# Kernel optimization log

Hardware: AMD Instinct MI355X
Metric: run time of the kernel (lower is better)

## Reference

```python
import jax, jax.numpy as jnp
import numpy as np


def _fft2c(x, axes):
    # fftshift(fft2(ifftshift(x), norm='ortho'))
    return jnp.fft.fftshift(
        jnp.fft.fft2(jnp.fft.ifftshift(x, axes=axes), axes=axes, norm='ortho'),
        axes=axes)


def _warp(img, flow):
    # img: [Nx,Ny] complex, flow: [Nx,Ny,2] (displacements along x,y)
    # Dense equivalent of the sparse bilinear motion matrix apply.
    Nx, Ny = img.shape
    gx = jnp.arange(Nx, dtype=flow.dtype)[:, None]
    gy = jnp.arange(Ny, dtype=flow.dtype)[None, :]
    x = jnp.clip(gx + flow[:, :, 0], 0.0, Nx - 1)
    y = jnp.clip(gy + flow[:, :, 1], 0.0, Ny - 1)
    x0 = jnp.clip(jnp.floor(x), 0, Nx - 2).astype(jnp.int32)
    y0 = jnp.clip(jnp.floor(y), 0, Ny - 2).astype(jnp.int32)
    wx = x - x0
    wy = y - y0
    x1 = x0 + 1
    y1 = y0 + 1
    v00 = img[x0, y0]
    v01 = img[x0, y1]
    v10 = img[x1, y0]
    v11 = img[x1, y1]
    return ((1 - wx) * (1 - wy)) * v00 + ((1 - wx) * wy) * v01 \
         + (wx * (1 - wy)) * v10 + (wx * wy) * v11


def setup_inputs() -> dict:
    key = jax.random.key(0)
    k = jax.random.split(key, 6)
    Nx, Ny, Nc, Nt = 256, 256, 16, 24
    return {
        'image_real': jax.random.normal(k[0], (Nx, Ny), dtype=jnp.float32),
        'image_imag': jax.random.normal(k[1], (Nx, Ny), dtype=jnp.float32),
        'mask': jax.random.uniform(k[2], (Nx, Ny, Nc, Nt), dtype=jnp.float32),
        'smaps_real': jax.random.normal(k[3], (Nx, Ny, Nc), dtype=jnp.float32),
        'smaps_imag': jax.random.normal(k[4], (Nx, Ny, Nc), dtype=jnp.float32),
        'flow': jax.random.normal(k[5], (Nx, Ny, 2, Nt), dtype=jnp.float32) * 2.0,
    }


def reference(image_real, image_imag, mask, smaps_real, smaps_imag, flow):
    img = image_real + 1j * image_imag            # [Nx,Ny]
    smaps = smaps_real + 1j * smaps_imag          # [Nx,Ny,Nc]
    flow_t = jnp.moveaxis(flow, -1, 0)            # [Nt,Nx,Ny,2]
    warped = jax.vmap(_warp, in_axes=(None, 0))(img, flow_t)   # [Nt,Nx,Ny]
    coil = warped[:, :, :, None] * smaps[None]    # [Nt,Nx,Ny,Nc]
    k = _fft2c(coil, axes=(1, 2))                 # [Nt,Nx,Ny,Nc]
    mask_t = jnp.moveaxis(mask, -1, 0)            # [Nt,Nx,Ny,Nc]
    out = jnp.sum(k * mask_t, axis=0)             # [Nx,Ny,Nc] complex
    # stack real/imag for a real-valued output (complex not in dtype enum)
    return jnp.stack([out.real, out.imag], axis=0)  # [2,Nx,Ny,Nc]
```

## Files before the change

### kernel.cpp

```cpp
#include <hip/hip_runtime.h>
#include <math.h>

#define NCD 16
#define NTD 24
#define NPIX 65536

struct c32 { float x, y; };

__device__ __forceinline__ c32 cadd(c32 a, c32 b){ return {a.x+b.x, a.y+b.y}; }
__device__ __forceinline__ c32 csub(c32 a, c32 b){ return {a.x-b.x, a.y-b.y}; }
__device__ __forceinline__ c32 cmul(c32 a, c32 b){ return {a.x*b.x - a.y*b.y, a.x*b.y + a.y*b.x}; }
__device__ __forceinline__ c32 cnegi(c32 a){ return {a.y, -a.x}; }

__device__ __forceinline__ unsigned short f2h(float f) {
  return __builtin_bit_cast(unsigned short, (_Float16)f);
}
__device__ __forceinline__ float h2f(unsigned short s) {
  return (float)__builtin_bit_cast(_Float16, s);
}

__constant__ float W16R_[16] = {
  1.0f, 0.9238795325f, 0.7071067812f, 0.3826834324f,
  0.0f,-0.3826834324f,-0.7071067812f,-0.9238795325f,
 -1.0f,-0.9238795325f,-0.7071067812f,-0.3826834324f,
  0.0f, 0.3826834324f, 0.7071067812f, 0.9238795325f };
__constant__ float W16I_[16] = {
  0.0f,-0.3826834324f,-0.7071067812f,-0.9238795325f,
 -1.0f,-0.9238795325f,-0.7071067812f,-0.3826834324f,
  0.0f, 0.3826834324f, 0.7071067812f, 0.9238795325f,
  1.0f, 0.9238795325f, 0.7071067812f, 0.3826834324f };

__device__ __forceinline__ int revmap(int p) { return ((p & 3) << 2) | (p >> 2); }

__device__ __forceinline__ void dft16(c32 v[16]) {
  c32 y[16];
#pragma unroll
  for (int j = 0; j < 4; ++j) {
    c32 a = v[j], b = v[j+4], c = v[j+8], d = v[j+12];
    c32 t0 = cadd(a,c), t1 = csub(a,c), t2 = cadd(b,d), t3 = cnegi(csub(b,d));
    y[j] = cadd(t0,t2);
    if (j == 0) {
      y[4]  = cadd(t1,t3);
      y[8]  = csub(t0,t2);
      y[12] = csub(t1,t3);
    } else {
      c32 w1 = {W16R_[j],        W16I_[j]};
      c32 w2 = {W16R_[(2*j)&15], W16I_[(2*j)&15]};
      c32 w3 = {W16R_[(3*j)&15], W16I_[(3*j)&15]};
      y[4+j]  = cmul(cadd(t1,t3), w1);
      y[8+j]  = cmul(csub(t0,t2), w2);
      y[12+j] = cmul(csub(t1,t3), w3);
    }
  }
#pragma unroll
  for (int q = 0; q < 4; ++q) {
    c32 a = y[4*q], b = y[4*q+1], c = y[4*q+2], d = y[4*q+3];
    c32 t0 = cadd(a,c), t1 = csub(a,c), t2 = cadd(b,d), t3 = cnegi(csub(b,d));
    v[4*q+0] = cadd(t0,t2);
    v[4*q+1] = cadd(t1,t3);
    v[4*q+2] = csub(t0,t2);
    v[4*q+3] = csub(t1,t3);
  }
}

__device__ __forceinline__ void fft256(c32 v[16], const c32 tw[16], c32* lds,
                                       int g, int lane) {
  dft16(v);
#pragma unroll
  for (int p = 0; p < 16; ++p) v[p] = cmul(v[p], tw[p]);
  __syncthreads();
#pragma unroll
  for (int p = 0; p < 16; ++p) {
    int k1 = revmap(p);
    lds[g*256 + k1*16 + (lane ^ k1)] = v[p];
  }
  __syncthreads();
#pragma unroll
  for (int j = 0; j < 16; ++j)
    v[j] = lds[g*256 + lane*16 + (j ^ lane)];
  dft16(v);
}

__global__ __launch_bounds__(256) void kS(const float* __restrict__ sre,
                                          const float* __restrict__ sim,
                                          c32* __restrict__ smapsT) {
  __shared__ float lre[16*260];
  __shared__ float lim[16*260];
  int nx = blockIdx.x, tid = threadIdx.x;
#pragma unroll
  for (int it = 0; it < 16; ++it) {
    int e = it*256 + tid;
    int ny = e >> 4, c = e & 15;
    lre[c*260 + ny] = sre[(size_t)nx*4096 + e];
    lim[c*260 + ny] = sim[(size_t)nx*4096 + e];
  }
  __syncthreads();
#pragma unroll
  for (int c = 0; c < 16; ++c) {
    c32 v = { lre[c*260 + tid], lim[c*260 + tid] };
    smapsT[(size_t)c*NPIX + nx*256 + tid] = v;
  }
}

__global__ __launch_bounds__(256) void kW(const float* __restrict__ ire,
                                          const float* __restrict__ iim,
                                          const float* __restrict__ flow,
                                          c32* __restrict__ w) {
  __shared__ float fl[256*49];
  int nx = blockIdx.x, tid = threadIdx.x;
  const float* src = flow + (size_t)nx*12288;
#pragma unroll
  for (int it = 0; it < 48; ++it) {
    int e = it*256 + tid;
    fl[(e/48)*49 + (e%48)] = src[e];
  }
  __syncthreads();
  int ny = tid;
  float s = ((nx + ny) & 1) ? -1.0f : 1.0f;
  for (int t = 0; t < NTD; ++t) {
    float fx = fl[ny*49 + t];
    float fy = fl[ny*49 + 24 + t];
    float xf = fminf(fmaxf((float)nx + fx, 0.0f), 255.0f);
    float yf = fminf(fmaxf((float)ny + fy, 0.0f), 255.0f);
    float x0f = fminf(floorf(xf), 254.0f);
    float y0f = fminf(floorf(yf), 254.0f);
    int i00 = (int)x0f * 256 + (int)y0f;
    float wx = xf - x0f, wy = yf - y0f;
    float w00 = (1.f-wx)*(1.f-wy), w01 = (1.f-wx)*wy;
    float w10 = wx*(1.f-wy),       w11 = wx*wy;
    float re = w00*ire[i00] + w01*ire[i00+1] + w10*ire[i00+256] + w11*ire[i00+257];
    float im = w00*iim[i00] + w01*iim[i00+1] + w10*iim[i00+256] + w11*iim[i00+257];
    c32 v = { re*s, im*s };
    w[(size_t)t*NPIX + nx*256 + ny] = v;
  }
}

__global__ __launch_bounds__(256) void kM(const float* __restrict__ mask,
                                          unsigned int* __restrict__ maskTh,
                                          int t0, int chunkT) {
  __shared__ unsigned short lm[256*49];
  int ky = blockIdx.x, c0 = blockIdx.y*2, tid = threadIdx.x;
  int nct = 2*chunkT;
  int total = 256*nct;
  for (int e = tid; e < total; e += 256) {
    int kx = e / nct, ctl = e - kx*nct;
    int hi = (ctl >= chunkT) ? 1 : 0;
    int cc = c0 + hi;
    int tt = t0 + ctl - hi*chunkT;
    lm[kx*49 + ctl] = f2h(mask[(size_t)kx*98304 + ky*384 + cc*24 + tt]);
  }
  __syncthreads();
  int wtotal = nct*128;
  for (int e = tid; e < wtotal; e += 256) {
    int ctl = e >> 7;
    int posh = (e & 127) * 2;
    int hi = (ctl >= chunkT) ? 1 : 0;
    int cc = c0 + hi;
    int ltt = ctl - hi*chunkT;
    int kxa = ((posh & 15) << 4) | (posh >> 4);
    int kxb = (((posh+1) & 15) << 4) | ((posh+1) >> 4);
    unsigned int a = lm[kxa*49 + ctl], b = lm[kxb*49 + ctl];
    size_t base = (((((size_t)ltt*256 + ky)*16 + cc) << 8) + posh) >> 1;
    maskTh[base] = a | (b << 16);
  }
}

__global__ __launch_bounds__(256) void kA(const c32* __restrict__ w,
                                          const c32* __restrict__ smapsT,
                                          unsigned int* __restrict__ Y1h, int t0) {
  __shared__ c32 lds[4096];
  __shared__ unsigned int stage[4096];
  int tid = threadIdx.x, g = tid >> 4, lane = tid & 15;
  int lt = blockIdx.y, t = t0 + lt;
  int nx0 = blockIdx.x*16, nx = nx0 + g;
  int c0 = blockIdx.z*4;

  c32 wr[16];
  const c32* wrow = w + (size_t)t*NPIX + nx*256;
#pragma unroll
  for (int n1 = 0; n1 < 16; ++n1) wr[n1] = wrow[n1*16 + lane];

  c32 tw[16];
#pragma unroll
  for (int p = 0; p < 16; ++p) {
    int k1 = revmap(p);
    float ang = -6.283185307179586f * (float)(lane * k1) * (1.0f/256.0f);
    float sv, cv; __sincosf(ang, &sv, &cv);
    tw[p].x = cv; tw[p].y = sv;
  }

  for (int ci = 0; ci < 4; ++ci) {
    int c = c0 + ci;
    const c32* srow = smapsT + (size_t)c*NPIX + nx*256;
    c32 v[16];
#pragma unroll
    for (int n1 = 0; n1 < 16; ++n1) v[n1] = cmul(wr[n1], srow[n1*16 + lane]);
    fft256(v, tw, lds, g, lane);
#pragma unroll
    for (int p = 0; p < 16; ++p) {
      int ky = lane + 16*revmap(p);
      unsigned int pk = (unsigned int)f2h(v[p].x)
                      | ((unsigned int)f2h(v[p].y) << 16);
      stage[ky*16 + (g ^ lane)] = pk;
    }
    __syncthreads();
    unsigned int* dst = Y1h + (((size_t)lt*16 + c) << 16) + nx0;
#pragma unroll
    for (int it = 0; it < 16; ++it) {
      int e = it*256 + tid;
      int ky = e >> 4, j = e & 15;
      dst[(size_t)ky*256 + j] = stage[ky*16 + (j ^ (ky & 15))];
    }
  }
}

__global__ __launch_bounds__(256) void kB(const unsigned int* __restrict__ Y1h,
                                          const unsigned int* __restrict__ maskTh,
                                          float* __restrict__ out,
                                          int chunkT, int accum) {
  __shared__ c32 lds[4096];
  int tid = threadIdx.x, g = tid >> 4, lane = tid & 15;
  int ci = g & 3, tp = g >> 2;
  int cq = blockIdx.x, ky = blockIdx.y;
  int c = cq*4 + ci;

  c32 tw[16];
#pragma unroll
  for (int p = 0; p < 16; ++p) {
    int k1 = revmap(p);
    float ang = -6.283185307179586f * (float)(lane * k1) * (1.0f/256.0f);
    float sv, cv; __sincosf(ang, &sv, &cv);
    tw[p].x = cv; tw[p].y = sv;
  }

  c32 acc[16];
#pragma unroll
  for (int p = 0; p < 16; ++p) { acc[p].x = 0.f; acc[p].y = 0.f; }
  float wsc = (((lane + ky) & 1) ? -1.0f : 1.0f) * (1.0f/256.0f);

  int iters = (chunkT + 3) >> 2;
  for (int ii = 0; ii < iters; ++ii) {
    int lt = tp + 4*ii;
    bool act = lt < chunkT;
    int lts = act ? lt : 0;
    const unsigned int* row = Y1h + ((size_t)(lts*16 + c)*256 + ky)*256;
    const unsigned int* mp = maskTh
        + (((((size_t)lts*256 + ky)*16 + c) << 8) >> 1) + lane*8;
    unsigned int mu[8];
#pragma unroll
    for (int q = 0; q < 8; ++q) mu[q] = mp[q];
    c32 v[16];
#pragma unroll
    for (int n1 = 0; n1 < 16; ++n1) {
      unsigned int uu = row[n1*16 + lane];
      v[n1].x = h2f((unsigned short)(uu & 0xffffu));
      v[n1].y = h2f((unsigned short)(uu >> 16));
    }
    fft256(v, tw, lds, g, lane);
    if (act) {
#pragma unroll
      for (int p = 0; p < 16; ++p) {
        int j = revmap(p);
        unsigned int um = mu[j >> 1];
        unsigned short us = (j & 1) ? (unsigned short)(um >> 16)
                                    : (unsigned short)(um & 0xffffu);
        float m = h2f(us) * wsc;
        acc[p].x += v[p].x * m;
        acc[p].y += v[p].y * m;
      }
    }
  }
  __syncthreads();
#pragma unroll
  for (int p = 0; p < 16; ++p) lds[g*256 + p*16 + lane] = acc[p];
  __syncthreads();
  int kx = tid;
  int lane2 = kx & 15, pp = revmap(kx >> 4);
  float vre[4], vim[4];
#pragma unroll
  for (int c2 = 0; c2 < 4; ++c2) {
    float sx = 0.f, sy = 0.f;
#pragma unroll
    for (int t2 = 0; t2 < 4; ++t2) {
      c32 a = lds[(t2*4 + c2)*256 + pp*16 + lane2];
      sx += a.x; sy += a.y;
    }
    vre[c2] = sx; vim[c2] = sy;
  }
  size_t o = (((size_t)kx << 8) + ky)*16 + cq*4;
  float4* pre = (float4*)(out + o);
  float4* pim = (float4*)(out + (size_t)NPIX*NCD + o);
  float4 R = {vre[0], vre[1], vre[2], vre[3]};
  float4 I = {vim[0], vim[1], vim[2], vim[3]};
  if (accum) {
    float4 r0 = *pre, i0 = *pim;
    R.x += r0.x; R.y += r0.y; R.z += r0.z; R.w += r0.w;
    I.x += i0.x; I.y += i0.y; I.z += i0.z; I.w += i0.w;
  }
  *pre = R; *pim = I;
}

extern "C" void kernel_launch(void* const* d_in, const int* in_sizes, int n_in,
                              void* d_out, int out_size, void* d_ws, size_t ws_size,
                              hipStream_t stream) {
  const float* ire  = (const float*)d_in[0];
  const float* iim  = (const float*)d_in[1];
  const float* mask = (const float*)d_in[2];
  const float* sre  = (const float*)d_in[3];
  const float* sim  = (const float*)d_in[4];
  const float* flow = (const float*)d_in[5];
  float* out = (float*)d_out;

  char* ws = (char*)d_ws;
  const size_t smapsT_b = (size_t)NCD * NPIX * sizeof(c32);
  const size_t w_b      = (size_t)NTD * NPIX * sizeof(c32);
  c32* smapsT = (c32*)ws;
  c32* wbuf   = (c32*)(ws + smapsT_b);
  size_t base = smapsT_b + w_b;
  size_t rem  = (ws_size > base) ? ws_size - base : 0;

  const size_t maskT_per_t = (size_t)NPIX * NCD * 2;
  const size_t y1_per_t    = (size_t)NCD * NPIX * 4;
  int chunk = 1;
  const int cands[8] = {24, 12, 8, 6, 4, 3, 2, 1};
  for (int i = 0; i < 8; ++i) {
    if ((size_t)cands[i] * (maskT_per_t + y1_per_t) <= rem) { chunk = cands[i]; break; }
  }
  unsigned int* maskTh = (unsigned int*)(ws + base);
  unsigned int* Y1h    = (unsigned int*)(ws + base + (size_t)chunk * maskT_per_t);

  kS<<<256, 256, 0, stream>>>(sre, sim, smapsT);
  kW<<<256, 256, 0, stream>>>(ire, iim, flow, wbuf);
  for (int t0 = 0; t0 < NTD; t0 += chunk) {
    kM<<<dim3(256, 8), 256, 0, stream>>>(mask, maskTh, t0, chunk);
    kA<<<dim3(16, chunk, 4), 256, 0, stream>>>(wbuf, smapsT, Y1h, t0);
    kB<<<dim3(4, 256), 256, 0, stream>>>(Y1h, maskTh, out, chunk, t0 > 0 ? 1 : 0);
  }
}
```

Measured before the change: 329.8 us.

## Store intermediates and twiddles in fp16, prefetch next rows, add occupancy bounds

Smaps and warped image intermediates are now stored as packed fp16 pairs, halving their global traffic. kA's LDS transpose now also uses packed fp16 with a padded stride. Twiddles are held as packed halves to cut register use, and both kA and kB prefetch the next coil or time row into registers before the current FFT. Launch bounds now request 4 blocks per CU. Together these aim to cut memory traffic and register pressure and to hide load latency, at the cost of more fp16 rounding error in the intermediates and twiddles.

New measurement: 499.5 us. 1.51x slower.

```diff
diff --git a/kernel.cpp b/kernel.cpp
--- a/kernel.cpp
+++ b/kernel.cpp
@@ -17,6 +17,13 @@
 }
 __device__ __forceinline__ float h2f(unsigned short s) {
   return (float)__builtin_bit_cast(_Float16, s);
+}
+__device__ __forceinline__ unsigned int pk2(c32 v) {
+  return (unsigned int)f2h(v.x) | ((unsigned int)f2h(v.y) << 16);
+}
+__device__ __forceinline__ c32 up2(unsigned int u) {
+  c32 r; r.x = h2f((unsigned short)(u & 0xffffu)); r.y = h2f((unsigned short)(u >> 16));
+  return r;
 }
 
 __constant__ float W16R_[16] = {
@@ -63,11 +70,11 @@
   }
 }
 
-__device__ __forceinline__ void fft256(c32 v[16], const c32 tw[16], c32* lds,
-                                       int g, int lane) {
+__device__ __forceinline__ void fft256(c32 v[16], const unsigned int twh[16],
+                                       c32* lds, int g, int lane) {
   dft16(v);
 #pragma unroll
-  for (int p = 0; p < 16; ++p) v[p] = cmul(v[p], tw[p]);
+  for (int p = 0; p < 16; ++p) v[p] = cmul(v[p], up2(twh[p]));
   __syncthreads();
 #pragma unroll
   for (int p = 0; p < 16; ++p) {
@@ -81,9 +88,27 @@
   dft16(v);
 }
 
+__device__ __forceinline__ void fft256h(c32 v[16], const unsigned int twh[16],
+                                        unsigned int* ldsu, int g, int lane) {
+  dft16(v);
+#pragma unroll
+  for (int p = 0; p < 16; ++p) v[p] = cmul(v[p], up2(twh[p]));
+  __syncthreads();
+#pragma unroll
+  for (int p = 0; p < 16; ++p) {
+    int k1 = revmap(p);
+    ldsu[g*272 + k1*17 + lane] = pk2(v[p]);
+  }
+  __syncthreads();
+#pragma unroll
+  for (int j = 0; j < 16; ++j)
+    v[j] = up2(ldsu[g*272 + lane*17 + j]);
+  dft16(v);
+}
+
 __global__ __launch_bounds__(256) void kS(const float* __restrict__ sre,
                                           const float* __restrict__ sim,
-                                          c32* __restrict__ smapsT) {
+                                          unsigned int* __restrict__ smapsTh) {
   __shared__ float lre[16*260];
   __shared__ float lim[16*260];
   int nx = blockIdx.x, tid = threadIdx.x;
@@ -98,14 +123,14 @@
 #pragma unroll
   for (int c = 0; c < 16; ++c) {
     c32 v = { lre[c*260 + tid], lim[c*260 + tid] };
-    smapsT[(size_t)c*NPIX + nx*256 + tid] = v;
+    smapsTh[(size_t)c*NPIX + nx*256 + tid] = pk2(v);
   }
 }
 
 __global__ __launch_bounds__(256) void kW(const float* __restrict__ ire,
                                           const float* __restrict__ iim,
                                           const float* __restrict__ flow,
-                                          c32* __restrict__ w) {
+                                          unsigned int* __restrict__ wh) {
   __shared__ float fl[256*49];
   int nx = blockIdx.x, tid = threadIdx.x;
   const float* src = flow + (size_t)nx*12288;
@@ -131,7 +156,7 @@
     float re = w00*ire[i00] + w01*ire[i00+1] + w10*ire[i00+256] + w11*ire[i00+257];
     float im = w00*iim[i00] + w01*iim[i00+1] + w10*iim[i00+256] + w11*iim[i00+257];
     c32 v = { re*s, im*s };
-    w[(size_t)t*NPIX + nx*256 + ny] = v;
+    wh[(size_t)t*NPIX + nx*256 + ny] = pk2(v);
   }
 }
 
@@ -165,43 +190,53 @@
   }
 }
 
-__global__ __launch_bounds__(256) void kA(const c32* __restrict__ w,
-                                          const c32* __restrict__ smapsT,
-                                          unsigned int* __restrict__ Y1h, int t0) {
-  __shared__ c32 lds[4096];
+__global__ __launch_bounds__(256, 4) void kA(const unsigned int* __restrict__ wh,
+                                             const unsigned int* __restrict__ smapsTh,
+                                             unsigned int* __restrict__ Y1h, int t0) {
+  __shared__ unsigned int fftws[4352];
   __shared__ unsigned int stage[4096];
   int tid = threadIdx.x, g = tid >> 4, lane = tid & 15;
   int lt = blockIdx.y, t = t0 + lt;
   int nx0 = blockIdx.x*16, nx = nx0 + g;
   int c0 = blockIdx.z*4;
 
-  c32 wr[16];
-  const c32* wrow = w + (size_t)t*NPIX + nx*256;
+  unsigned int wr[16];
+  const unsigned int* wrow = wh + (size_t)t*NPIX + nx*256;
 #pragma unroll
   for (int n1 = 0; n1 < 16; ++n1) wr[n1] = wrow[n1*16 + lane];
 
-  c32 tw[16];
+  unsigned int twh[16];
 #pragma unroll
   for (int p = 0; p < 16; ++p) {
     int k1 = revmap(p);
     float ang = -6.283185307179586f * (float)(lane * k1) * (1.0f/256.0f);
     float sv, cv; __sincosf(ang, &sv, &cv);
-    tw[p].x = cv; tw[p].y = sv;
+    c32 tw; tw.x = cv; tw.y = sv;
+    twh[p] = pk2(tw);
+  }
+
+  unsigned int su[16];
+  {
+    const unsigned int* srow = smapsTh + (size_t)c0*NPIX + nx*256;
+#pragma unroll
+    for (int n1 = 0; n1 < 16; ++n1) su[n1] = srow[n1*16 + lane];
   }
 
   for (int ci = 0; ci < 4; ++ci) {
     int c = c0 + ci;
-    const c32* srow = smapsT + (size_t)c*NPIX + nx*256;
     c32 v[16];
 #pragma unroll
-    for (int n1 = 0; n1 < 16; ++n1) v[n1] = cmul(wr[n1], srow[n1*16 + lane]);
-    fft256(v, tw, lds, g, lane);
+    for (int n1 = 0; n1 < 16; ++n1) v[n1] = cmul(up2(wr[n1]), up2(su[n1]));
+    if (ci < 3) {
+      const unsigned int* srow = smapsTh + (size_t)(c + 1)*NPIX + nx*256;
+#pragma unroll
+      for (int n1 = 0; n1 < 16; ++n1) su[n1] = srow[n1*16 + lane];
+    }
+    fft256h(v, twh, fftws, g, lane);
 #pragma unroll
     for (int p = 0; p < 16; ++p) {
       int ky = lane + 16*revmap(p);
-      unsigned int pk = (unsigned int)f2h(v[p].x)
-                      | ((unsigned int)f2h(v[p].y) << 16);
-      stage[ky*16 + (g ^ lane)] = pk;
+      stage[ky*16 + (g ^ lane)] = pk2(v[p]);
     }
     __syncthreads();
     unsigned int* dst = Y1h + (((size_t)lt*16 + c) << 16) + nx0;
@@ -214,23 +249,24 @@
   }
 }
 
-__global__ __launch_bounds__(256) void kB(const unsigned int* __restrict__ Y1h,
-                                          const unsigned int* __restrict__ maskTh,
-                                          float* __restrict__ out,
-                                          int chunkT, int accum) {
+__global__ __launch_bounds__(256, 4) void kB(const unsigned int* __restrict__ Y1h,
+                                             const unsigned int* __restrict__ maskTh,
+                                             float* __restrict__ out,
+                                             int chunkT, int accum) {
   __shared__ c32 lds[4096];
   int tid = threadIdx.x, g = tid >> 4, lane = tid & 15;
   int ci = g & 3, tp = g >> 2;
   int cq = blockIdx.x, ky = blockIdx.y;
   int c = cq*4 + ci;
 
-  c32 tw[16];
+  unsigned int twh[16];
 #pragma unroll
   for (int p = 0; p < 16; ++p) {
     int k1 = revmap(p);
     float ang = -6.283185307179586f * (float)(lane * k1) * (1.0f/256.0f);
     float sv, cv; __sincosf(ang, &sv, &cv);
-    tw[p].x = cv; tw[p].y = sv;
+    c32 tw; tw.x = cv; tw.y = sv;
+    twh[p] = pk2(tw);
   }
 
   c32 acc[16];
@@ -239,11 +275,19 @@
   float wsc = (((lane + ky) & 1) ? -1.0f : 1.0f) * (1.0f/256.0f);
 
   int iters = (chunkT + 3) >> 2;
+  unsigned int u[16];
+#pragma unroll
+  for (int n1 = 0; n1 < 16; ++n1) u[n1] = 0;
+  if (tp < chunkT) {
+    const unsigned int* row = Y1h + ((size_t)(tp*16 + c)*256 + ky)*256;
+#pragma unroll
+    for (int n1 = 0; n1 < 16; ++n1) u[n1] = row[n1*16 + lane];
+  }
+
   for (int ii = 0; ii < iters; ++ii) {
     int lt = tp + 4*ii;
     bool act = lt < chunkT;
     int lts = act ? lt : 0;
-    const unsigned int* row = Y1h + ((size_t)(lts*16 + c)*256 + ky)*256;
     const unsigned int* mp = maskTh
         + (((((size_t)lts*256 + ky)*16 + c) << 8) >> 1) + lane*8;
     unsigned int mu[8];
@@ -251,12 +295,14 @@
     for (int q = 0; q < 8; ++q) mu[q] = mp[q];
     c32 v[16];
 #pragma unroll
-    for (int n1 = 0; n1 < 16; ++n1) {
-      unsigned int uu = row[n1*16 + lane];
-      v[n1].x = h2f((unsigned short)(uu & 0xffffu));
-      v[n1].y = h2f((unsigned short)(uu >> 16));
-    }
-    fft256(v, tw, lds, g, lane);
+    for (int n1 = 0; n1 < 16; ++n1) v[n1] = up2(u[n1]);
+    int ltn = tp + 4*(ii+1);
+    if (ltn < chunkT) {
+      const unsigned int* row = Y1h + ((size_t)(ltn*16 + c)*256 + ky)*256;
+#pragma unroll
+      for (int n1 = 0; n1 < 16; ++n1) u[n1] = row[n1*16 + lane];
+    }
+    fft256(v, twh, lds, g, lane);
     if (act) {
 #pragma unroll
       for (int p = 0; p < 16; ++p) {
@@ -312,10 +358,10 @@
   float* out = (float*)d_out;
 
   char* ws = (char*)d_ws;
-  const size_t smapsT_b = (size_t)NCD * NPIX * sizeof(c32);
-  const size_t w_b      = (size_t)NTD * NPIX * sizeof(c32);
-  c32* smapsT = (c32*)ws;
-  c32* wbuf   = (c32*)(ws + smapsT_b);
+  const size_t smapsT_b = (size_t)NCD * NPIX * 4;
+  const size_t w_b      = (size_t)NTD * NPIX * 4;
+  unsigned int* smapsTh = (unsigned int*)ws;
+  unsigned int* whbuf   = (unsigned int*)(ws + smapsT_b);
   size_t base = smapsT_b + w_b;
   size_t rem  = (ws_size > base) ? ws_size - base : 0;
 
@@ -329,11 +375,11 @@
   unsigned int* maskTh = (unsigned int*)(ws + base);
   unsigned int* Y1h    = (unsigned int*)(ws + base + (size_t)chunk * maskT_per_t);
 
-  kS<<<256, 256, 0, stream>>>(sre, sim, smapsT);
-  kW<<<256, 256, 0, stream>>>(ire, iim, flow, wbuf);
+  kS<<<256, 256, 0, stream>>>(sre, sim, smapsTh);
+  kW<<<256, 256, 0, stream>>>(ire, iim, flow, whbuf);
   for (int t0 = 0; t0 < NTD; t0 += chunk) {
     kM<<<dim3(256, 8), 256, 0, stream>>>(mask, maskTh, t0, chunk);
-    kA<<<dim3(16, chunk, 4), 256, 0, stream>>>(wbuf, smapsT, Y1h, t0);
+    kA<<<dim3(16, chunk, 4), 256, 0, stream>>>(whbuf, smapsTh, Y1h, t0);
     kB<<<dim3(4, 256), 256, 0, stream>>>(Y1h, maskTh, out, chunk, t0 > 0 ? 1 : 0);
   }
 }
```
